# Kernel tuning notes

Hardware: AMD Instinct MI355X
Metric: run time of the kernel (lower is better)

## Reference

```python
import jax, jax.numpy as jnp
import numpy as np

N, T, ENC_H, ATT_H, DEC_H, OUT, SPK = 32, 4096, 512, 256, 512, 80, 64
ATT_RANGE = 10
KW = 31  # conv kernel width, padding 15


def softsign(x):
    return x / (1.0 + jnp.abs(x))


def setup_inputs() -> dict:
    key = jax.random.key(0)
    ks = jax.random.split(key, 20)
    lengths_enc = jax.random.randint(ks[0], (N,), 2048, T + 1)
    pos = jnp.arange(T)
    prev_attention = jax.random.uniform(ks[1], (N, T, 1), jnp.float32)
    # zero attention beyond valid length (so argmax lies within length, as in practice)
    prev_attention = prev_attention * (pos[None, :, None] < lengths_enc[:, None, None])
    s = 0.05
    inp = {
        "input_enc": jax.random.normal(ks[2], (N, T, ENC_H), jnp.float32),
        "input_dec": jax.random.normal(ks[3], (N, 1, OUT), jnp.float32),
        "prev_attention": prev_attention,
        "spkr_vec": jax.random.normal(ks[4], (N, 1, SPK), jnp.float32),
        "lengths_enc": lengths_enc,
        "speed": jax.random.uniform(ks[5], (N,), jnp.float32),
        # parameters (torch Linear: y = x @ W.T + b; we store W already transposed)
        "W_enc": jax.random.normal(ks[6], (ENC_H, ATT_H), jnp.float32) * s,
        "b_enc": jnp.zeros((ATT_H,), jnp.float32),
        "W_spkr": jax.random.normal(ks[7], (SPK, ATT_H), jnp.float32) * s,
        "conv_w": jax.random.normal(ks[8], (ATT_H, 1, KW), jnp.float32) * s,  # OIH
        "W_dec": jax.random.normal(ks[9], (DEC_H, ATT_H), jnp.float32) * s,
        "W_speed": jax.random.normal(ks[10], (1, ATT_H), jnp.float32) * s,
        "Wp1": jax.random.normal(ks[11], (OUT + SPK, 2 * DEC_H), jnp.float32) * s,
        "bp1": jnp.zeros((2 * DEC_H,), jnp.float32),
        "Wp2": jax.random.normal(ks[12], (2 * DEC_H, DEC_H), jnp.float32) * s,
        "bp2": jnp.zeros((DEC_H,), jnp.float32),
        "W_proj": jax.random.normal(ks[13], (ATT_H, 1), jnp.float32) * s,
        "b_proj": jnp.zeros((1,), jnp.float32),
    }
    return inp


def reference(input_enc, input_dec, prev_attention, spkr_vec, lengths_enc, speed,
              W_enc, b_enc, W_spkr, conv_w, W_dec, W_speed,
              Wp1, bp1, Wp2, bp2, W_proj, b_proj):
    # prenet (dropout = identity in eval mode)
    dec_in = jnp.concatenate([input_dec, spkr_vec], axis=-1)          # [N,1,OUT+SPK]
    h = jax.nn.relu(dec_in @ Wp1 + bp1)                               # [N,1,2*DEC_H]
    out_prenet = jax.nn.relu(h @ Wp2 + bp2)                           # [N,1,DEC_H]

    # biases (computed fresh, null_bias branch)
    att_bias_speed = (speed[:, None] @ W_speed)[:, None, :]           # [N,1,ATT_H]
    att_bias_enc = softsign(input_enc @ W_enc + b_enc)                # [N,T,ATT_H]
    att_bias_spkr = softsign(spkr_vec @ W_spkr)                       # [N,1,ATT_H]

    # location conv: [N,T,1] -> [N,1,T] -> conv(k=31,p=15) -> [N,ATT_H,T] -> [N,T,ATT_H]
    conv = jax.lax.conv_general_dilated(
        prev_attention.transpose(0, 2, 1), conv_w,
        window_strides=(1,), padding=[(15, 15)],
        dimension_numbers=("NCH", "OIH", "NCH"))
    in_att_prev_att = conv.transpose(0, 2, 1)                         # [N,T,ATT_H]

    in_att_dec = out_prenet @ W_dec                                   # [N,1,ATT_H]

    e = att_bias_enc + in_att_dec + att_bias_spkr + in_att_prev_att + att_bias_speed
    logit = jnp.tanh(e) @ W_proj + b_proj                             # [N,T,1]

    # windowed band mask around argmax of prev attention (no_grad in torch)
    max_idx = jnp.argmax(prev_attention[:, :, 0], axis=1)             # [N]
    lo = jnp.maximum(max_idx - (ATT_RANGE - 1), 0)
    hi = jnp.minimum(max_idx + (ATT_RANGE - 1), lengths_enc - 1)
    pos = jnp.arange(T)
    att_mask = ((pos[None, :] >= lo[:, None]) & (pos[None, :] <= hi[:, None]))
    att_mask = att_mask[:, :, None].astype(logit.dtype)               # [N,T,1]

    logit_max = jnp.max(logit, axis=1, keepdims=True)
    curr = jnp.exp(logit - logit_max) * att_mask
    denom = jnp.maximum(jnp.sum(jnp.abs(curr), axis=1, keepdims=True), 1e-12)
    return curr / denom
```

## Files before the change

### kernel.cpp

```cpp
#include <hip/hip_runtime.h>
#include <hip/hip_bf16.h>

#define NB     32
#define TLEN   4096
#define ENCH   512
#define ATTH   256
#define DECH   512
#define OUTD   80
#define SPKD   64
#define KW     31
#define ATTR   10

__global__ __launch_bounds__(1024) void prep_kernel(
    const float* __restrict__ pa,
    const float* __restrict__ input_dec,
    const float* __restrict__ spkr_vec,
    const float* __restrict__ speed,
    const float* __restrict__ Wp1,
    const float* __restrict__ bp1,
    const float* __restrict__ Wp2,
    const float* __restrict__ bp2,
    const float* __restrict__ W_dec,
    const float* __restrict__ W_spkr,
    const float* __restrict__ W_speed,
    float* __restrict__ out,
    int* __restrict__ ws_idx,
    float* __restrict__ ws_bias)
{
  const int n   = blockIdx.x;
  const int tid = threadIdx.x;

  __shared__ float s_dec[144];
  __shared__ float s_h1[1024];
  __shared__ float s_op[512];
  __shared__ __align__(16) float s_red[8 * 512];
  __shared__ float s_av[1024];
  __shared__ int   s_ai[1024];

  {
    float4* o4 = (float4*)(out + (size_t)n * TLEN);
    o4[tid] = make_float4(0.f, 0.f, 0.f, 0.f);
  }

  if (tid < OUTD)      s_dec[tid] = input_dec[n * OUTD + tid];
  else if (tid < 144)  s_dec[tid] = spkr_vec[n * SPKD + (tid - OUTD)];

  {
    const float* p = pa + (size_t)n * TLEN;
    float bv = -1.f; int bi = 0;
    #pragma unroll
    for (int k = 0; k < TLEN / 1024; k++) {
      int t = tid + k * 1024;
      float v = p[t];
      if (v > bv) { bv = v; bi = t; }
    }
    s_av[tid] = bv; s_ai[tid] = bi;
    __syncthreads();
    for (int s = 512; s > 0; s >>= 1) {
      if (tid < s) {
        float ov = s_av[tid + s]; int oi = s_ai[tid + s];
        float mv = s_av[tid];     int mi = s_ai[tid];
        if (ov > mv || (ov == mv && oi < mi)) { s_av[tid] = ov; s_ai[tid] = oi; }
      }
      __syncthreads();
    }
    if (tid == 0) ws_idx[n] = s_ai[0];
  }

  {
    float acc = bp1[tid];
    #pragma unroll 4
    for (int i = 0; i < 144; i++)
      acc = fmaf(s_dec[i], Wp1[i * 1024 + tid], acc);
    s_h1[tid] = fmaxf(acc, 0.f);
  }
  __syncthreads();

  {
    const int g = tid & 127, sl = tid >> 7;
    const int k0 = g * 4;
    float4 acc = make_float4(0.f, 0.f, 0.f, 0.f);
    for (int j = sl; j < 1024; j += 8) {
      float hv = s_h1[j];
      float4 w = *(const float4*)(Wp2 + (size_t)j * 512 + k0);
      acc.x = fmaf(hv, w.x, acc.x);
      acc.y = fmaf(hv, w.y, acc.y);
      acc.z = fmaf(hv, w.z, acc.z);
      acc.w = fmaf(hv, w.w, acc.w);
    }
    *(float4*)(s_red + sl * 512 + k0) = acc;
    __syncthreads();
    if (tid < 512) {
      float v = bp2[tid];
      #pragma unroll
      for (int s2 = 0; s2 < 8; s2++) v += s_red[s2 * 512 + tid];
      s_op[tid] = fmaxf(v, 0.f);
    }
    __syncthreads();
  }

  {
    const int c = tid & 255, sl = tid >> 8;
    float acc = 0.f;
    const int kb = sl * 128;
    #pragma unroll 4
    for (int k = kb; k < kb + 128; k++)
      acc = fmaf(s_op[k], W_dec[k * 256 + c], acc);
    s_red[sl * 256 + c] = acc;
    __syncthreads();
    if (tid < 256) {
      float b = s_red[tid] + s_red[256 + tid] + s_red[512 + tid] + s_red[768 + tid];
      float sp = 0.f;
      #pragma unroll 4
      for (int i = 0; i < 64; i++)
        sp = fmaf(s_dec[OUTD + i], W_spkr[i * 256 + tid], sp);
      sp = sp / (1.f + fabsf(sp));
      b += sp + speed[n] * W_speed[tid];
      ws_bias[n * 256 + tid] = b;
    }
  }
}

__global__ __launch_bounds__(256) void band_kernel(
    const float* __restrict__ input_enc,
    const float* __restrict__ pa,
    const int*   __restrict__ lengths,
    const float* __restrict__ W_enc,
    const float* __restrict__ b_enc,
    const float* __restrict__ conv_w,
    const float* __restrict__ W_proj,
    const int*   __restrict__ ws_idx,
    const float* __restrict__ ws_bias,
    float* __restrict__ ws_logits)
{
  const int n  = blockIdx.x;
  const int jb = blockIdx.y;
  const int tid = threadIdx.x;

  const int mi  = ws_idx[n];
  const int len = lengths[n];
  const int lo  = max(mi - (ATTR - 1), 0);
  const int hi  = min(mi + (ATTR - 1), len - 1);
  const int t0  = lo + jb * 4;

  __shared__ float s_enc[4][ENCH];
  __shared__ float s_pa[34];
  __shared__ float s_part[4][4];

  #pragma unroll
  for (int q = 0; q < 4; q++) {
    int t = t0 + q;
    bool valid = (t <= hi);
    const float* src = input_enc + ((size_t)n * TLEN + t) * ENCH;
    s_enc[q][tid]       = valid ? src[tid]       : 0.f;
    s_enc[q][tid + 256] = valid ? src[tid + 256] : 0.f;
  }
  if (tid < 34) {
    int idx = t0 - (KW / 2) + tid;
    s_pa[tid] = (idx >= 0 && idx < TLEN) ? pa[(size_t)n * TLEN + idx] : 0.f;
  }
  __syncthreads();

  const int c = tid;
  float a0 = 0.f, a1 = 0.f, a2 = 0.f, a3 = 0.f;
  #pragma unroll 8
  for (int i = 0; i < ENCH; i++) {
    float w = W_enc[i * 256 + c];
    a0 = fmaf(s_enc[0][i], w, a0);
    a1 = fmaf(s_enc[1][i], w, a1);
    a2 = fmaf(s_enc[2][i], w, a2);
    a3 = fmaf(s_enc[3][i], w, a3);
  }

  float c0 = 0.f, c1 = 0.f, c2 = 0.f, c3 = 0.f;
  #pragma unroll
  for (int k = 0; k < KW; k++) {
    float w = conv_w[c * KW + k];
    c0 = fmaf(s_pa[0 + k], w, c0);
    c1 = fmaf(s_pa[1 + k], w, c1);
    c2 = fmaf(s_pa[2 + k], w, c2);
    c3 = fmaf(s_pa[3 + k], w, c3);
  }

  const float be   = b_enc[c];
  const float bias = ws_bias[n * 256 + c];
  const float wp   = W_proj[c];

  float v[4];
  {
    float s0 = a0 + be; s0 = s0 / (1.f + fabsf(s0)); v[0] = tanhf(s0 + bias + c0) * wp;
    float s1 = a1 + be; s1 = s1 / (1.f + fabsf(s1)); v[1] = tanhf(s1 + bias + c1) * wp;
    float s2 = a2 + be; s2 = s2 / (1.f + fabsf(s2)); v[2] = tanhf(s2 + bias + c2) * wp;
    float s3 = a3 + be; s3 = s3 / (1.f + fabsf(s3)); v[3] = tanhf(s3 + bias + c3) * wp;
  }

  const int lane = tid & 63, wv = tid >> 6;
  #pragma unroll
  for (int q = 0; q < 4; q++) {
    float x = v[q];
    #pragma unroll
    for (int off = 32; off > 0; off >>= 1) x += __shfl_down(x, off);
    if (lane == 0) s_part[wv][q] = x;
  }
  __syncthreads();
  if (tid < 4) {
    float s = s_part[0][tid] + s_part[1][tid] + s_part[2][tid] + s_part[3][tid];
    int j = jb * 4 + tid;
    int t = t0 + tid;
    ws_logits[n * 20 + j] = (t <= hi) ? s : -__builtin_inff();
  }
}

__global__ __launch_bounds__(64) void softmax_kernel(
    const float* __restrict__ ws_logits,
    const int*   __restrict__ ws_idx,
    const int*   __restrict__ lengths,
    float* __restrict__ out)
{
  const int n = blockIdx.x;
  const int tid = threadIdx.x;
  const int mi  = ws_idx[n];
  const int len = lengths[n];
  const int lo  = max(mi - (ATTR - 1), 0);
  const int hi  = min(mi + (ATTR - 1), len - 1);

  float l = (tid < 20) ? ws_logits[n * 20 + tid] : -__builtin_inff();
  float m = l;
  #pragma unroll
  for (int off = 32; off > 0; off >>= 1) m = fmaxf(m, __shfl_down(m, off));
  m = __shfl(m, 0);
  float e = __expf(l - m);
  float s = e;
  #pragma unroll
  for (int off = 32; off > 0; off >>= 1) s += __shfl_down(s, off);
  s = __shfl(s, 0);

  int t = lo + tid;
  if (tid < 20 && t <= hi)
    out[(size_t)n * TLEN + t] = e / s;
}

extern "C" void kernel_launch(void* const* d_in, const int* in_sizes, int n_in,
                              void* d_out, int out_size, void* d_ws, size_t ws_size,
                              hipStream_t stream) {
  const float* input_enc = (const float*)d_in[0];
  const float* input_dec = (const float*)d_in[1];
  const float* pa        = (const float*)d_in[2];
  const float* spkr_vec  = (const float*)d_in[3];
  const int*   lengths   = (const int*)  d_in[4];
  const float* speed     = (const float*)d_in[5];
  const float* W_enc     = (const float*)d_in[6];
  const float* b_enc     = (const float*)d_in[7];
  const float* W_spkr    = (const float*)d_in[8];
  const float* conv_w    = (const float*)d_in[9];
  const float* W_dec     = (const float*)d_in[10];
  const float* W_speed   = (const float*)d_in[11];
  const float* Wp1       = (const float*)d_in[12];
  const float* bp1       = (const float*)d_in[13];
  const float* Wp2       = (const float*)d_in[14];
  const float* bp2       = (const float*)d_in[15];
  const float* W_proj    = (const float*)d_in[16];

  float* out = (float*)d_out;

  int*   ws_idx    = (int*)d_ws;
  float* ws_bias   = (float*)((char*)d_ws + 256);
  float* ws_logits = (float*)((char*)d_ws + 256 + NB * 256 * sizeof(float));

  hipLaunchKernelGGL(prep_kernel, dim3(NB), dim3(1024), 0, stream,
                     pa, input_dec, spkr_vec, speed, Wp1, bp1, Wp2, bp2,
                     W_dec, W_spkr, W_speed, out, ws_idx, ws_bias);

  hipLaunchKernelGGL(band_kernel, dim3(NB, 5), dim3(256), 0, stream,
                     input_enc, pa, lengths, W_enc, b_enc, conv_w, W_proj,
                     ws_idx, ws_bias, ws_logits);

  hipLaunchKernelGGL(softmax_kernel, dim3(NB), dim3(64), 0, stream,
                     ws_logits, ws_idx, lengths, out);
}
```

Before: 453.6 us.

## Fuse prep, band logits, and softmax into one per-batch kernel

Merges the three kernels into a single 1024-thread block per batch row. The argmax window, bias vector and logits stay in shared memory instead of going through workspace, and the band loop runs 5 groups of 4 timesteps sequentially inside the block. This removes two launches and the global round trips between them. In exchange the band work, which was spread over 160 blocks, is serialized within 32 blocks, so per-block latency rises.

Measured after the change: 507.5 us. 1.12x slower.

```diff
diff --git a/kernel.cpp b/kernel.cpp
--- a/kernel.cpp
+++ b/kernel.cpp
@@ -5,27 +5,30 @@
 #define TLEN   4096
 #define ENCH   512
 #define ATTH   256
-#define DECH   512
 #define OUTD   80
 #define SPKD   64
 #define KW     31
 #define ATTR   10
 
-__global__ __launch_bounds__(1024) void prep_kernel(
+__global__ __launch_bounds__(1024) void fused_kernel(
+    const float* __restrict__ input_enc,
+    const float* __restrict__ input_dec,
     const float* __restrict__ pa,
-    const float* __restrict__ input_dec,
     const float* __restrict__ spkr_vec,
+    const int*   __restrict__ lengths,
     const float* __restrict__ speed,
+    const float* __restrict__ W_enc,
+    const float* __restrict__ b_enc,
+    const float* __restrict__ W_spkr,
+    const float* __restrict__ conv_w,
+    const float* __restrict__ W_dec,
+    const float* __restrict__ W_speed,
     const float* __restrict__ Wp1,
     const float* __restrict__ bp1,
     const float* __restrict__ Wp2,
     const float* __restrict__ bp2,
-    const float* __restrict__ W_dec,
-    const float* __restrict__ W_spkr,
-    const float* __restrict__ W_speed,
-    float* __restrict__ out,
-    int* __restrict__ ws_idx,
-    float* __restrict__ ws_bias)
+    const float* __restrict__ W_proj,
+    float* __restrict__ out)
 {
   const int n   = blockIdx.x;
   const int tid = threadIdx.x;
@@ -36,11 +39,14 @@
   __shared__ __align__(16) float s_red[8 * 512];
   __shared__ float s_av[1024];
   __shared__ int   s_ai[1024];
-
-  {
-    float4* o4 = (float4*)(out + (size_t)n * TLEN);
-    o4[tid] = make_float4(0.f, 0.f, 0.f, 0.f);
-  }
+  __shared__ float s_bias[256];
+  __shared__ float s_enc[4][ENCH];
+  __shared__ float s_pa[52];
+  __shared__ float s_part[16];
+  __shared__ float s_logits[20];
+  __shared__ int   s_lo, s_hi;
+
+  ((float4*)(out + (size_t)n * TLEN))[tid] = make_float4(0.f, 0.f, 0.f, 0.f);
 
   if (tid < OUTD)      s_dec[tid] = input_dec[n * OUTD + tid];
   else if (tid < 144)  s_dec[tid] = spkr_vec[n * SPKD + (tid - OUTD)];
@@ -64,7 +70,11 @@
       }
       __syncthreads();
     }
-    if (tid == 0) ws_idx[n] = s_ai[0];
+    if (tid == 0) {
+      int mi = s_ai[0];
+      s_lo = max(mi - (ATTR - 1), 0);
+      s_hi = min(mi + (ATTR - 1), lengths[n] - 1);
+    }
   }
 
   {
@@ -75,6 +85,11 @@
     s_h1[tid] = fmaxf(acc, 0.f);
   }
   __syncthreads();
+
+  if (tid < 52) {
+    int idx = s_lo - (KW / 2) + tid;
+    s_pa[tid] = (idx >= 0 && idx < TLEN) ? pa[(size_t)n * TLEN + idx] : 0.f;
+  }
 
   {
     const int g = tid & 127, sl = tid >> 7;
@@ -115,129 +130,76 @@
       for (int i = 0; i < 64; i++)
         sp = fmaf(s_dec[OUTD + i], W_spkr[i * 256 + tid], sp);
       sp = sp / (1.f + fabsf(sp));
-      b += sp + speed[n] * W_speed[tid];
-      ws_bias[n * 256 + tid] = b;
-    }
-  }
-}
-
-__global__ __launch_bounds__(256) void band_kernel(
-    const float* __restrict__ input_enc,
-    const float* __restrict__ pa,
-    const int*   __restrict__ lengths,
-    const float* __restrict__ W_enc,
-    const float* __restrict__ b_enc,
-    const float* __restrict__ conv_w,
-    const float* __restrict__ W_proj,
-    const int*   __restrict__ ws_idx,
-    const float* __restrict__ ws_bias,
-    float* __restrict__ ws_logits)
-{
-  const int n  = blockIdx.x;
-  const int jb = blockIdx.y;
-  const int tid = threadIdx.x;
-
-  const int mi  = ws_idx[n];
-  const int len = lengths[n];
-  const int lo  = max(mi - (ATTR - 1), 0);
-  const int hi  = min(mi + (ATTR - 1), len - 1);
-  const int t0  = lo + jb * 4;
-
-  __shared__ float s_enc[4][ENCH];
-  __shared__ float s_pa[34];
-  __shared__ float s_part[4][4];
-
-  #pragma unroll
-  for (int q = 0; q < 4; q++) {
-    int t = t0 + q;
-    bool valid = (t <= hi);
-    const float* src = input_enc + ((size_t)n * TLEN + t) * ENCH;
-    s_enc[q][tid]       = valid ? src[tid]       : 0.f;
-    s_enc[q][tid + 256] = valid ? src[tid + 256] : 0.f;
-  }
-  if (tid < 34) {
-    int idx = t0 - (KW / 2) + tid;
-    s_pa[tid] = (idx >= 0 && idx < TLEN) ? pa[(size_t)n * TLEN + idx] : 0.f;
+      s_bias[tid] = b + sp + speed[n] * W_speed[tid];
+    }
   }
   __syncthreads();
 
-  const int c = tid;
-  float a0 = 0.f, a1 = 0.f, a2 = 0.f, a3 = 0.f;
-  #pragma unroll 8
-  for (int i = 0; i < ENCH; i++) {
-    float w = W_enc[i * 256 + c];
-    a0 = fmaf(s_enc[0][i], w, a0);
-    a1 = fmaf(s_enc[1][i], w, a1);
-    a2 = fmaf(s_enc[2][i], w, a2);
-    a3 = fmaf(s_enc[3][i], w, a3);
-  }
-
-  float c0 = 0.f, c1 = 0.f, c2 = 0.f, c3 = 0.f;
-  #pragma unroll
-  for (int k = 0; k < KW; k++) {
-    float w = conv_w[c * KW + k];
-    c0 = fmaf(s_pa[0 + k], w, c0);
-    c1 = fmaf(s_pa[1 + k], w, c1);
-    c2 = fmaf(s_pa[2 + k], w, c2);
-    c3 = fmaf(s_pa[3 + k], w, c3);
-  }
-
-  const float be   = b_enc[c];
-  const float bias = ws_bias[n * 256 + c];
-  const float wp   = W_proj[c];
-
-  float v[4];
-  {
-    float s0 = a0 + be; s0 = s0 / (1.f + fabsf(s0)); v[0] = tanhf(s0 + bias + c0) * wp;
-    float s1 = a1 + be; s1 = s1 / (1.f + fabsf(s1)); v[1] = tanhf(s1 + bias + c1) * wp;
-    float s2 = a2 + be; s2 = s2 / (1.f + fabsf(s2)); v[2] = tanhf(s2 + bias + c2) * wp;
-    float s3 = a3 + be; s3 = s3 / (1.f + fabsf(s3)); v[3] = tanhf(s3 + bias + c3) * wp;
-  }
-
-  const int lane = tid & 63, wv = tid >> 6;
-  #pragma unroll
-  for (int q = 0; q < 4; q++) {
-    float x = v[q];
-    #pragma unroll
-    for (int off = 32; off > 0; off >>= 1) x += __shfl_down(x, off);
-    if (lane == 0) s_part[wv][q] = x;
-  }
-  __syncthreads();
-  if (tid < 4) {
-    float s = s_part[0][tid] + s_part[1][tid] + s_part[2][tid] + s_part[3][tid];
-    int j = jb * 4 + tid;
-    int t = t0 + tid;
-    ws_logits[n * 20 + j] = (t <= hi) ? s : -__builtin_inff();
-  }
-}
-
-__global__ __launch_bounds__(64) void softmax_kernel(
-    const float* __restrict__ ws_logits,
-    const int*   __restrict__ ws_idx,
-    const int*   __restrict__ lengths,
-    float* __restrict__ out)
-{
-  const int n = blockIdx.x;
-  const int tid = threadIdx.x;
-  const int mi  = ws_idx[n];
-  const int len = lengths[n];
-  const int lo  = max(mi - (ATTR - 1), 0);
-  const int hi  = min(mi + (ATTR - 1), len - 1);
-
-  float l = (tid < 20) ? ws_logits[n * 20 + tid] : -__builtin_inff();
-  float m = l;
-  #pragma unroll
-  for (int off = 32; off > 0; off >>= 1) m = fmaxf(m, __shfl_down(m, off));
-  m = __shfl(m, 0);
-  float e = __expf(l - m);
-  float s = e;
-  #pragma unroll
-  for (int off = 32; off > 0; off >>= 1) s += __shfl_down(s, off);
-  s = __shfl(s, 0);
-
-  int t = lo + tid;
-  if (tid < 20 && t <= hi)
-    out[(size_t)n * TLEN + t] = e / s;
+  const int lo = s_lo, hi = s_hi;
+  const int q  = tid >> 8;
+  const int c  = tid & 255;
+  const float be = b_enc[c];
+  const float wp = W_proj[c];
+  const float bs = s_bias[c];
+
+  for (int g = 0; g < 5; g++) {
+    {
+      int e0 = tid, e1 = tid + 1024;
+      int q0 = e0 >> 9, i0 = e0 & 511;
+      int q1 = e1 >> 9, i1 = e1 & 511;
+      int t0 = lo + g * 4 + q0;
+      int t1 = lo + g * 4 + q1;
+      s_enc[q0][i0] = (t0 <= hi) ? input_enc[((size_t)n * TLEN + t0) * ENCH + i0] : 0.f;
+      s_enc[q1][i1] = (t1 <= hi) ? input_enc[((size_t)n * TLEN + t1) * ENCH + i1] : 0.f;
+    }
+    __syncthreads();
+
+    float a0 = 0.f, a1 = 0.f;
+    #pragma unroll 8
+    for (int i = 0; i < ENCH; i += 2) {
+      a0 = fmaf(s_enc[q][i],     W_enc[i * 256 + c],       a0);
+      a1 = fmaf(s_enc[q][i + 1], W_enc[(i + 1) * 256 + c], a1);
+    }
+    float a = a0 + a1;
+
+    const int slot = g * 4 + q;
+    float cv = 0.f;
+    #pragma unroll
+    for (int k = 0; k < KW; k++)
+      cv = fmaf(s_pa[slot + k], conv_w[c * KW + k], cv);
+
+    float ss = a + be;
+    ss = ss / (1.f + fabsf(ss));
+    float v = tanhf(ss + bs + cv) * wp;
+
+    #pragma unroll
+    for (int off = 32; off > 0; off >>= 1) v += __shfl_down(v, off);
+    if ((tid & 63) == 0) s_part[tid >> 6] = v;
+    __syncthreads();
+    if (tid < 4) {
+      float s = s_part[tid * 4] + s_part[tid * 4 + 1]
+              + s_part[tid * 4 + 2] + s_part[tid * 4 + 3];
+      int t = lo + g * 4 + tid;
+      s_logits[g * 4 + tid] = (t <= hi) ? s : -__builtin_inff();
+    }
+    __syncthreads();
+  }
+
+  if (tid < 64) {
+    float l = (tid < 20) ? s_logits[tid] : -__builtin_inff();
+    float m = l;
+    #pragma unroll
+    for (int off = 32; off > 0; off >>= 1) m = fmaxf(m, __shfl_down(m, off));
+    m = __shfl(m, 0);
+    float e = __expf(l - m);
+    float s = e;
+    #pragma unroll
+    for (int off = 32; off > 0; off >>= 1) s += __shfl_down(s, off);
+    s = __shfl(s, 0);
+    int t = lo + tid;
+    if (tid < 20 && t <= hi)
+      out[(size_t)n * TLEN + t] = e / s;
+  }
 }
 
 extern "C" void kernel_launch(void* const* d_in, const int* in_sizes, int n_in,
@@ -263,18 +225,8 @@
 
   float* out = (float*)d_out;
 
-  int*   ws_idx    = (int*)d_ws;
-  float* ws_bias   = (float*)((char*)d_ws + 256);
-  float* ws_logits = (float*)((char*)d_ws + 256 + NB * 256 * sizeof(float));
-
-  hipLaunchKernelGGL(prep_kernel, dim3(NB), dim3(1024), 0, stream,
-                     pa, input_dec, spkr_vec, speed, Wp1, bp1, Wp2, bp2,
-                     W_dec, W_spkr, W_speed, out, ws_idx, ws_bias);
-
-  hipLaunchKernelGGL(band_kernel, dim3(NB, 5), dim3(256), 0, stream,
-                     input_enc, pa, lengths, W_enc, b_enc, conv_w, W_proj,
-                     ws_idx, ws_bias, ws_logits);
-
-  hipLaunchKernelGGL(softmax_kernel, dim3(NB), dim3(64), 0, stream,
-                     ws_logits, ws_idx, lengths, out);
+  hipLaunchKernelGGL(fused_kernel, dim3(NB), dim3(1024), 0, stream,
+                     input_enc, input_dec, pa, spkr_vec, lengths, speed,
+                     W_enc, b_enc, W_spkr, conv_w, W_dec, W_speed,
+                     Wp1, bp1, Wp2, bp2, W_proj, out);
 }
```
